# Kernel tuning notes

Hardware: AMD Instinct MI355X
Metric: run time of the kernel (lower is better)

## Reference

```python
import jax, jax.numpy as jnp
import numpy as np

EPS = 1e-5  # BatchNorm eps (eval mode, uses running stats)


def _conv1x1(x, W, b):
    # x: [B,C,H,W], W: [O,C], b: [O] -> [B,O,H,W]
    return jnp.einsum('bchw,oc->bohw', x, W) + b[None, :, None, None]


def setup_inputs() -> dict:
    key = jax.random.key(0)
    ks = jax.random.split(key, 13)
    B, C, M, N = 16, 512, 64, 64
    CR = C // 2
    s = 0.02
    return {
        'x': jax.random.normal(ks[0], (B, C, M, N), dtype=jnp.float32),
        'Wq': jax.random.normal(ks[1], (CR, C), dtype=jnp.float32) * s,
        'bq': jax.random.normal(ks[2], (CR,), dtype=jnp.float32) * s,
        'Wk': jax.random.normal(ks[3], (CR, C), dtype=jnp.float32) * s,
        'bk': jax.random.normal(ks[4], (CR,), dtype=jnp.float32) * s,
        'Wv': jax.random.normal(ks[5], (CR, C), dtype=jnp.float32) * s,
        'bv': jax.random.normal(ks[6], (CR,), dtype=jnp.float32) * s,
        'Wr': jax.random.normal(ks[7], (C, CR), dtype=jnp.float32) * s,
        'br': jax.random.normal(ks[8], (C,), dtype=jnp.float32) * s,
        'gamma': jax.random.normal(ks[9], (C,), dtype=jnp.float32) * 0.1 + 1.0,
        'beta': jax.random.normal(ks[10], (C,), dtype=jnp.float32) * 0.1,
        'running_mean': jax.random.normal(ks[11], (C,), dtype=jnp.float32) * 0.1,
        'running_var': jax.random.uniform(ks[12], (C,), dtype=jnp.float32, minval=0.5, maxval=1.5),
    }


def reference(x, Wq, bq, Wk, bk, Wv, bv, Wr, br, gamma, beta, running_mean, running_var):
    b, c, m, n = x.shape
    cr = Wq.shape[0]
    # 1x1-conv QKV projections
    Q = _conv1x1(x, Wq, bq).reshape(b * cr, m, n)
    K = _conv1x1(x, Wk, bk).reshape(b * cr, m, n)
    V = _conv1x1(x, Wv, bv).reshape(b * cr, m, n)
    # per-channel spatial attention over rows: [b*cr, m, m]
    corr = jnp.einsum('gik,gjk->gij', Q, K)
    attn = jax.nn.softmax(corr, axis=-1)
    y = jnp.einsum('gij,gjn->gin', attn, V).reshape(b, cr, m, n)
    # reconstruct: 1x1 conv + BatchNorm (eval mode) + residual
    y = _conv1x1(y, Wr, br)
    inv = gamma / jnp.sqrt(running_var + EPS)
    y = y * inv[None, :, None, None] + (beta - running_mean * inv)[None, :, None, None]
    return y + x
```

## Files before the change

### kernel.cpp

```cpp
#include <hip/hip_runtime.h>

typedef __attribute__((ext_vector_type(8))) short bf16x8;
typedef __attribute__((ext_vector_type(4))) short bf16x4;
typedef __attribute__((ext_vector_type(4))) float f32x4;

#define DEVI static __device__ __forceinline__

DEVI unsigned short f2b(float f) {
  union { float f; unsigned u; } v; v.f = f;
  unsigned r = v.u + 0x7fffu + ((v.u >> 16) & 1u);
  return (unsigned short)(r >> 16);
}

typedef const __attribute__((address_space(1))) void* gas1_t;
typedef __attribute__((address_space(3))) void* las3_t;
#define GL16(g, l) __builtin_amdgcn_global_load_lds((gas1_t)(g), (las3_t)(l), 16, 0, 0)
#define LDSOFF(p) ((unsigned)(size_t)(__attribute__((address_space(3))) void*)(p))

#define WAITVM(N) asm volatile("s_waitcnt vmcnt(" #N ")" ::: "memory")
#define WAITLGKM  asm volatile("s_waitcnt lgkmcnt(0)" ::: "memory")
#define SCHEDBAR  __builtin_amdgcn_sched_barrier(0)

#define OFF_WQKV  0ull
#define OFF_WR    786432ull
#define OFF_BQKV  1048576ull
#define OFF_SCALE 1051648ull
#define OFF_OFF2  1053696ull
#define OFF_XT    2097152ull
#define OFF_Y     35651584ull
#define OFF_Q     69206016ull

__global__ __launch_bounds__(256) void k_xt(
    const float* __restrict__ x, unsigned short* __restrict__ xt,
    const float* __restrict__ Wq, const float* __restrict__ bq,
    const float* __restrict__ Wk, const float* __restrict__ bk,
    const float* __restrict__ Wv, const float* __restrict__ bv,
    const float* __restrict__ Wr, const float* __restrict__ br,
    const float* __restrict__ gamma, const float* __restrict__ beta,
    const float* __restrict__ rm, const float* __restrict__ rv,
    unsigned short* __restrict__ wqkv, unsigned short* __restrict__ wrb,
    float* __restrict__ bqkv, float* __restrict__ scale, float* __restrict__ off2)
{
  __shared__ unsigned short tile[64][72];
  const int t = threadIdx.x;
  const int bid = blockIdx.x + blockIdx.y * 64 + blockIdx.z * 512;

  if (bid < 1536) {
    int i = bid * 256 + t;
    if (i < 768 * 512) {
      int o = i >> 9, c = i & 511;
      float v = (o < 256) ? Wq[o * 512 + c] : (o < 512 ? Wk[(o - 256) * 512 + c] : Wv[(o - 512) * 512 + c]);
      wqkv[i] = f2b(v);
    }
    if (i < 512 * 256) wrb[i] = f2b(Wr[i]);
    if (i < 768) bqkv[i] = (i < 256) ? bq[i] : (i < 512 ? bk[i - 256] : bv[i - 512]);
    if (i < 512) {
      float inv = gamma[i] * rsqrtf(rv[i] + 1e-5f);
      scale[i] = inv;
      off2[i] = (br[i] - rm[i]) * inv + beta[i];
    }
  }

  const int b = blockIdx.z, c0 = blockIdx.y * 64, s0 = blockIdx.x * 64;
  const int r = t >> 2, cc = (t & 3) * 16;
  const float* src = x + ((size_t)b * 512 + c0 + r) * 4096 + s0 + cc;
  #pragma unroll
  for (int j = 0; j < 16; j += 4) {
    float4 v = *(const float4*)(src + j);
    tile[r][cc + j + 0] = f2b(v.x);
    tile[r][cc + j + 1] = f2b(v.y);
    tile[r][cc + j + 2] = f2b(v.z);
    tile[r][cc + j + 3] = f2b(v.w);
  }
  __syncthreads();
  unsigned short* dst = xt + ((size_t)b * 4096 + s0 + r) * 512 + c0 + cc;
  bf16x8 o0, o1;
  #pragma unroll
  for (int j = 0; j < 8; ++j) { o0[j] = tile[cc + j][r]; o1[j] = tile[cc + 8 + j][r]; }
  *(bf16x8*)(dst) = o0;
  *(bf16x8*)(dst + 8) = o1;
}

__global__ __launch_bounds__(256) void k_qkv(
    const unsigned short* __restrict__ xt, const unsigned short* __restrict__ wqkv,
    const float* __restrict__ bqkv, unsigned short* __restrict__ qkv)
{
  __shared__ unsigned short lds[2][2][8192];
  const int b = blockIdx.z, o0 = blockIdx.y * 128, s0 = blockIdx.x * 128;
  const int t = threadIdx.x, w = t >> 6, l = t & 63;
  const int wm = w >> 1, wn = w & 1, lr = l & 15;
  const int lkE = (l >> 4) * 8;
  const int swE = (lr & 7) * 8;
  const int cp = (t & 7) ^ ((t >> 3) & 7);

  const unsigned short* Ag = wqkv + (size_t)(o0 + (t >> 3)) * 512 + cp * 8;
  const unsigned short* Bg = xt + ((size_t)b * 4096 + s0 + (t >> 3)) * 512 + cp * 8;

  const f32x4 z = {0.f, 0.f, 0.f, 0.f};
  f32x4 acc[4][4];
  #pragma unroll
  for (int i = 0; i < 4; ++i)
    #pragma unroll
    for (int j = 0; j < 4; ++j) acc[i][j] = z;

#define STG_Q(st, kt) do { \
    _Pragma("unroll") \
    for (int j = 0; j < 4; ++j) { \
      GL16(Ag + (kt) * 64 + j * 32 * 512, (char*)&lds[st][0][0] + j * 4096 + t * 16); \
      GL16(Bg + (kt) * 64 + j * 32 * 512, (char*)&lds[st][1][0] + j * 4096 + t * 16); \
    } \
  } while (0)

#define CMP_Q(st) do { \
    const unsigned short* A  = &lds[st][0][0]; \
    const unsigned short* Bl = &lds[st][1][0]; \
    bf16x8 af[2][4], bfr[2][4]; \
    _Pragma("unroll") \
    for (int kc = 0; kc < 2; ++kc) { \
      const int kidx = (kc * 32 + lkE) ^ swE; \
      _Pragma("unroll") \
      for (int mi = 0; mi < 4; ++mi) af[kc][mi] = *(const bf16x8*)(A + (wm * 64 + mi * 16 + lr) * 64 + kidx); \
      _Pragma("unroll") \
      for (int ni = 0; ni < 4; ++ni) bfr[kc][ni] = *(const bf16x8*)(Bl + (wn * 64 + ni * 16 + lr) * 64 + kidx); \
    } \
    _Pragma("unroll") \
    for (int kc = 0; kc < 2; ++kc) \
      _Pragma("unroll") \
      for (int mi = 0; mi < 4; ++mi) \
        _Pragma("unroll") \
        for (int ni = 0; ni < 4; ++ni) \
          acc[mi][ni] = __builtin_amdgcn_mfma_f32_16x16x32_bf16(af[kc][mi], bfr[kc][ni], acc[mi][ni], 0, 0, 0); \
  } while (0)

  STG_Q(0, 0); STG_Q(1, 1);
  #pragma unroll
  for (int kt = 0; kt < 7; ++kt) {
    WAITVM(8);
    __builtin_amdgcn_s_barrier(); SCHEDBAR;
    CMP_Q(kt & 1);
    __builtin_amdgcn_s_barrier(); SCHEDBAR;
    if (kt + 2 < 8) STG_Q(kt & 1, kt + 2);
  }
  WAITVM(0);
  __builtin_amdgcn_s_barrier(); SCHEDBAR;
  CMP_Q(1);

  #pragma unroll
  for (int mi = 0; mi < 4; ++mi) {
    #pragma unroll
    for (int reg = 0; reg < 4; ++reg) {
      const int o = o0 + wm * 64 + mi * 16 + (l >> 4) * 4 + reg;
      const float bias = bqkv[o];
      const size_t base = (size_t)(o >> 8) * 16777216ull + ((size_t)b * 256 + (o & 255)) * 4096;
      #pragma unroll
      for (int ni = 0; ni < 4; ++ni) {
        const int s = s0 + wn * 64 + ni * 16 + lr;
        qkv[base + s] = f2b(acc[mi][ni][reg] + bias);
      }
    }
  }
#undef STG_Q
#undef CMP_Q
}

__global__ __launch_bounds__(256) void k_attn(const unsigned short* __restrict__ qkv,
                                              unsigned short* __restrict__ yout)
{
  __shared__ unsigned short Vt[64][80];
  __shared__ unsigned short P[4][16][80];
  const int g = blockIdx.x;
  const unsigned short* qg = qkv + (size_t)g * 4096;
  const unsigned short* kg = qkv + 16777216ull + (size_t)g * 4096;
  const unsigned short* vg = qkv + 33554432ull + (size_t)g * 4096;
  const int t = threadIdx.x, w = t >> 6, l = t & 63;
  const int lr = l & 15, lk = (l >> 4) * 8;

  {
    const int j = t >> 2, c0 = (t & 3) * 16;
    bf16x8 a = *(const bf16x8*)(vg + j * 64 + c0);
    bf16x8 bb = *(const bf16x8*)(vg + j * 64 + c0 + 8);
    #pragma unroll
    for (int jj = 0; jj < 8; ++jj) { Vt[c0 + jj][j] = a[jj]; Vt[c0 + 8 + jj][j] = bb[jj]; }
  }

  const f32x4 z = {0.f, 0.f, 0.f, 0.f};
  bf16x8 qf[2];
  #pragma unroll
  for (int kc = 0; kc < 2; ++kc) qf[kc] = *(const bf16x8*)(qg + (w * 16 + lr) * 64 + kc * 32 + lk);
  f32x4 accS[4] = {z, z, z, z};
  __builtin_amdgcn_s_setprio(1);
  #pragma unroll
  for (int jt = 0; jt < 4; ++jt)
    #pragma unroll
    for (int kc = 0; kc < 2; ++kc) {
      bf16x8 kf = *(const bf16x8*)(kg + (jt * 16 + lr) * 64 + kc * 32 + lk);
      accS[jt] = __builtin_amdgcn_mfma_f32_16x16x32_bf16(qf[kc], kf, accS[jt], 0, 0, 0);
    }
  __builtin_amdgcn_s_setprio(0);

  #pragma unroll
  for (int reg = 0; reg < 4; ++reg) {
    float mx = fmaxf(fmaxf(accS[0][reg], accS[1][reg]), fmaxf(accS[2][reg], accS[3][reg]));
    #pragma unroll
    for (int m = 1; m < 16; m <<= 1) mx = fmaxf(mx, __shfl_xor(mx, m, 64));
    float e0 = __expf(accS[0][reg] - mx), e1 = __expf(accS[1][reg] - mx);
    float e2 = __expf(accS[2][reg] - mx), e3 = __expf(accS[3][reg] - mx);
    float sm = e0 + e1 + e2 + e3;
    #pragma unroll
    for (int m = 1; m < 16; m <<= 1) sm += __shfl_xor(sm, m, 64);
    const float rs = 1.f / sm;
    const int row = (l >> 4) * 4 + reg;
    P[w][row][0 * 16 + lr] = f2b(e0 * rs);
    P[w][row][1 * 16 + lr] = f2b(e1 * rs);
    P[w][row][2 * 16 + lr] = f2b(e2 * rs);
    P[w][row][3 * 16 + lr] = f2b(e3 * rs);
  }
  __syncthreads();

  bf16x8 pf[2];
  #pragma unroll
  for (int kc = 0; kc < 2; ++kc) pf[kc] = *(const bf16x8*)(&P[w][lr][kc * 32 + lk]);
  f32x4 accY[4] = {z, z, z, z};
  __builtin_amdgcn_s_setprio(1);
  #pragma unroll
  for (int nt = 0; nt < 4; ++nt)
    #pragma unroll
    for (int kc = 0; kc < 2; ++kc) {
      bf16x8 vf = *(const bf16x8*)(&Vt[nt * 16 + lr][kc * 32 + lk]);
      accY[nt] = __builtin_amdgcn_mfma_f32_16x16x32_bf16(pf[kc], vf, accY[nt], 0, 0, 0);
    }
  __builtin_amdgcn_s_setprio(0);

  unsigned short* yg = yout + (size_t)g * 4096;
  #pragma unroll
  for (int nt = 0; nt < 4; ++nt)
    #pragma unroll
    for (int reg = 0; reg < 4; ++reg) {
      const int i = w * 16 + (l >> 4) * 4 + reg;
      yg[i * 64 + nt * 16 + lr] = f2b(accY[nt][reg]);
    }
}

__global__ __launch_bounds__(256) void k_recon(
    const unsigned short* __restrict__ y, const unsigned short* __restrict__ wrb,
    const float* __restrict__ scale, const float* __restrict__ off2,
    const float* __restrict__ x, float* __restrict__ out)
{
  __shared__ unsigned short Albuf[2][8192];
  __shared__ unsigned short Blbuf[2][8192];
  const int b = blockIdx.z, o0 = blockIdx.y * 128, s0 = blockIdx.x * 128;
  const int t = threadIdx.x, w = t >> 6, l = t & 63;
  const int wm = w >> 1, wn = w & 1, lr = l & 15, g = l >> 4;
  const int lkE = g * 8;
  const int swE = (lr & 7) * 8;
  const int cp = (t & 7) ^ ((t >> 3) & 7);

  const unsigned short* Ag = wrb + (size_t)(o0 + (t >> 3)) * 256 + cp * 8;
  const unsigned short* Bg = y + ((size_t)b * 256 + (t >> 2)) * 4096 + s0 + (t & 3) * 32;
  const int bwbase = (t >> 4) * 1024 + (t & 3) * 256 + ((t >> 2) & 3) * 32;
  const int trbase = g * 2048 + wn * 512 + lr * 8;

  const f32x4 z = {0.f, 0.f, 0.f, 0.f};
  f32x4 acc[4][4];
  #pragma unroll
  for (int i = 0; i < 4; ++i)
    #pragma unroll
    for (int j = 0; j < 4; ++j) acc[i][j] = z;

  uint4 br0, br1, br2, br3;

#define ASTG(st, kt) do { \
    _Pragma("unroll") \
    for (int j = 0; j < 4; ++j) \
      GL16(Ag + (kt) * 64 + j * 32 * 256, (char*)&Albuf[st][0] + j * 4096 + t * 16); \
  } while (0)

#define BLOAD(kt) do { \
    br0 = *(const uint4*)(Bg + (size_t)(kt) * 64 * 4096 + 0); \
    br1 = *(const uint4*)(Bg + (size_t)(kt) * 64 * 4096 + 8); \
    br2 = *(const uint4*)(Bg + (size_t)(kt) * 64 * 4096 + 16); \
    br3 = *(const uint4*)(Bg + (size_t)(kt) * 64 * 4096 + 24); \
  } while (0)

#define BWRITE(st) do { \
    char* bp_ = (char*)&Blbuf[st][0] + bwbase; \
    *(uint4*)(bp_ + 0)   = br0; \
    *(uint4*)(bp_ + 16)  = br1; \
    *(uint4*)(bp_ + 128) = br2; \
    *(uint4*)(bp_ + 144) = br3; \
  } while (0)

#define TR2(dst, k0, k1) do { \
    bf16x4 t0_, t1_; \
    asm volatile("ds_read_b64_tr_b16 %0, %1 offset:" #k0 : "=v"(t0_) : "v"(ta)); \
    asm volatile("ds_read_b64_tr_b16 %0, %1 offset:" #k1 : "=v"(t1_) : "v"(ta)); \
    (dst) = __builtin_shufflevector(t0_, t1_, 0, 1, 2, 3, 4, 5, 6, 7); \
  } while (0)

#define CMP_R(st) do { \
    const unsigned short* A = &Albuf[st][0]; \
    unsigned ta = LDSOFF(&Blbuf[st][0]) + (unsigned)trbase; \
    bf16x8 af[2][4], bfr[2][4]; \
    _Pragma("unroll") \
    for (int kc = 0; kc < 2; ++kc) { \
      const int kidx = (kc * 32 + lkE) ^ swE; \
      _Pragma("unroll") \
      for (int mi = 0; mi < 4; ++mi) af[kc][mi] = *(const bf16x8*)(A + (wm * 64 + mi * 16 + lr) * 64 + kidx); \
    } \
    TR2(bfr[0][0], 0, 1024);    TR2(bfr[0][1], 128, 1152); \
    TR2(bfr[0][2], 256, 1280);  TR2(bfr[0][3], 384, 1408); \
    TR2(bfr[1][0], 8192, 9216); TR2(bfr[1][1], 8320, 9344); \
    TR2(bfr[1][2], 8448, 9472); TR2(bfr[1][3], 8576, 9600); \
    WAITLGKM; SCHEDBAR; \
    _Pragma("unroll") \
    for (int kc = 0; kc < 2; ++kc) \
      _Pragma("unroll") \
      for (int mi = 0; mi < 4; ++mi) \
        _Pragma("unroll") \
        for (int ni = 0; ni < 4; ++ni) \
          acc[mi][ni] = __builtin_amdgcn_mfma_f32_16x16x32_bf16(af[kc][mi], bfr[kc][ni], acc[mi][ni], 0, 0, 0); \
  } while (0)

  ASTG(0, 0); BLOAD(0); ASTG(1, 1);
  WAITVM(4);
  BWRITE(0); BLOAD(1);
  WAITLGKM;
  __builtin_amdgcn_s_barrier(); SCHEDBAR;
  CMP_R(0);
  __builtin_amdgcn_s_barrier(); SCHEDBAR;
  ASTG(0, 2);
  WAITVM(4);
  BWRITE(1); BLOAD(2);
  WAITLGKM;
  __builtin_amdgcn_s_barrier(); SCHEDBAR;
  CMP_R(1);
  __builtin_amdgcn_s_barrier(); SCHEDBAR;
  ASTG(1, 3);
  WAITVM(4);
  BWRITE(0); BLOAD(3);
  WAITLGKM;
  __builtin_amdgcn_s_barrier(); SCHEDBAR;
  CMP_R(0);
  __builtin_amdgcn_s_barrier(); SCHEDBAR;
  WAITVM(0);
  BWRITE(1);
  WAITLGKM;
  __builtin_amdgcn_s_barrier(); SCHEDBAR;
  CMP_R(1);

  const int lrow = (l >> 4) * 4;
  float xr0[16], xr1[16];

#define XLOAD(dstarr, mi) do { \
    _Pragma("unroll") \
    for (int reg = 0; reg < 4; ++reg) { \
      const int o_ = o0 + wm * 64 + (mi) * 16 + lrow + reg; \
      const size_t base_ = ((size_t)b * 512 + o_) * 4096; \
      _Pragma("unroll") \
      for (int ni = 0; ni < 4; ++ni) \
        dstarr[reg * 4 + ni] = x[base_ + s0 + wn * 64 + ni * 16 + lr]; \
    } \
  } while (0)

#define XSTORE(srcarr, mi) do { \
    _Pragma("unroll") \
    for (int reg = 0; reg < 4; ++reg) { \
      const int o_ = o0 + wm * 64 + (mi) * 16 + lrow + reg; \
      const float sc_ = scale[o_], of_ = off2[o_]; \
      const size_t base_ = ((size_t)b * 512 + o_) * 4096; \
      _Pragma("unroll") \
      for (int ni = 0; ni < 4; ++ni) { \
        const size_t idx_ = base_ + s0 + wn * 64 + ni * 16 + lr; \
        out[idx_] = acc[mi][ni][reg] * sc_ + of_ + srcarr[reg * 4 + ni]; \
      } \
    } \
  } while (0)

  XLOAD(xr0, 0);
  XLOAD(xr1, 1); SCHEDBAR;
  XSTORE(xr0, 0);
  XLOAD(xr0, 2); SCHEDBAR;
  XSTORE(xr1, 1);
  XLOAD(xr1, 3); SCHEDBAR;
  XSTORE(xr0, 2);
  XSTORE(xr1, 3);
#undef XLOAD
#undef XSTORE
#undef ASTG
#undef BLOAD
#undef BWRITE
#undef TR2
#undef CMP_R
}

extern "C" void kernel_launch(void* const* d_in, const int* in_sizes, int n_in,
                              void* d_out, int out_size, void* d_ws, size_t ws_size,
                              hipStream_t stream)
{
  const float* x     = (const float*)d_in[0];
  const float* Wq    = (const float*)d_in[1];
  const float* bq    = (const float*)d_in[2];
  const float* Wk    = (const float*)d_in[3];
  const float* bk    = (const float*)d_in[4];
  const float* Wv    = (const float*)d_in[5];
  const float* bv    = (const float*)d_in[6];
  const float* Wr    = (const float*)d_in[7];
  const float* br    = (const float*)d_in[8];
  const float* gamma = (const float*)d_in[9];
  const float* beta  = (const float*)d_in[10];
  const float* rm    = (const float*)d_in[11];
  const float* rv    = (const float*)d_in[12];

  char* ws = (char*)d_ws;
  unsigned short* wqkv  = (unsigned short*)(ws + OFF_WQKV);
  unsigned short* wrb   = (unsigned short*)(ws + OFF_WR);
  float* bqkv  = (float*)(ws + OFF_BQKV);
  float* scale = (float*)(ws + OFF_SCALE);
  float* off2  = (float*)(ws + OFF_OFF2);
  unsigned short* xt  = (unsigned short*)(ws + OFF_XT);
  unsigned short* yb  = (unsigned short*)(ws + OFF_Y);
  unsigned short* qkv = (unsigned short*)(ws + OFF_Q);
  float* out = (float*)d_out;

  hipLaunchKernelGGL(k_xt, dim3(64, 8, 16), dim3(256), 0, stream,
                     x, xt, Wq, bq, Wk, bk, Wv, bv, Wr, br, gamma, beta, rm, rv,
                     wqkv, wrb, bqkv, scale, off2);
  hipLaunchKernelGGL(k_qkv, dim3(32, 6, 16), dim3(256), 0, stream, xt, wqkv, bqkv, qkv);
  hipLaunchKernelGGL(k_attn, dim3(4096), dim3(256), 0, stream, qkv, yb);
  hipLaunchKernelGGL(k_recon, dim3(32, 4, 16), dim3(256), 0, stream, yb, wrb, scale, off2, x, out);
}
```

Measured before the change: 196.0 us.

## Fuse x transpose and bf16 conversion into QKV GEMM via LDS transpose reads

```diff
diff --git a/kernel.cpp b/kernel.cpp
--- a/kernel.cpp
+++ b/kernel.cpp
@@ -10,6 +10,9 @@
   union { float f; unsigned u; } v; v.f = f;
   unsigned r = v.u + 0x7fffu + ((v.u >> 16) & 1u);
   return (unsigned short)(r >> 16);
+}
+DEVI unsigned pk2(float lo, float hi) {
+  return (unsigned)f2b(lo) | ((unsigned)f2b(hi) << 16);
 }
 
 typedef const __attribute__((address_space(1))) void* gas1_t;
@@ -26,12 +29,10 @@
 #define OFF_BQKV  1048576ull
 #define OFF_SCALE 1051648ull
 #define OFF_OFF2  1053696ull
-#define OFF_XT    2097152ull
 #define OFF_Y     35651584ull
 #define OFF_Q     69206016ull
 
-__global__ __launch_bounds__(256) void k_xt(
-    const float* __restrict__ x, unsigned short* __restrict__ xt,
+__global__ __launch_bounds__(256) void k_prep(
     const float* __restrict__ Wq, const float* __restrict__ bq,
     const float* __restrict__ Wk, const float* __restrict__ bk,
     const float* __restrict__ Wv, const float* __restrict__ bv,
@@ -41,60 +42,38 @@
     unsigned short* __restrict__ wqkv, unsigned short* __restrict__ wrb,
     float* __restrict__ bqkv, float* __restrict__ scale, float* __restrict__ off2)
 {
-  __shared__ unsigned short tile[64][72];
-  const int t = threadIdx.x;
-  const int bid = blockIdx.x + blockIdx.y * 64 + blockIdx.z * 512;
-
-  if (bid < 1536) {
-    int i = bid * 256 + t;
-    if (i < 768 * 512) {
-      int o = i >> 9, c = i & 511;
-      float v = (o < 256) ? Wq[o * 512 + c] : (o < 512 ? Wk[(o - 256) * 512 + c] : Wv[(o - 512) * 512 + c]);
-      wqkv[i] = f2b(v);
-    }
-    if (i < 512 * 256) wrb[i] = f2b(Wr[i]);
-    if (i < 768) bqkv[i] = (i < 256) ? bq[i] : (i < 512 ? bk[i - 256] : bv[i - 512]);
-    if (i < 512) {
-      float inv = gamma[i] * rsqrtf(rv[i] + 1e-5f);
-      scale[i] = inv;
-      off2[i] = (br[i] - rm[i]) * inv + beta[i];
-    }
-  }
-
-  const int b = blockIdx.z, c0 = blockIdx.y * 64, s0 = blockIdx.x * 64;
-  const int r = t >> 2, cc = (t & 3) * 16;
-  const float* src = x + ((size_t)b * 512 + c0 + r) * 4096 + s0 + cc;
-  #pragma unroll
-  for (int j = 0; j < 16; j += 4) {
-    float4 v = *(const float4*)(src + j);
-    tile[r][cc + j + 0] = f2b(v.x);
-    tile[r][cc + j + 1] = f2b(v.y);
-    tile[r][cc + j + 2] = f2b(v.z);
-    tile[r][cc + j + 3] = f2b(v.w);
-  }
-  __syncthreads();
-  unsigned short* dst = xt + ((size_t)b * 4096 + s0 + r) * 512 + c0 + cc;
-  bf16x8 o0, o1;
-  #pragma unroll
-  for (int j = 0; j < 8; ++j) { o0[j] = tile[cc + j][r]; o1[j] = tile[cc + 8 + j][r]; }
-  *(bf16x8*)(dst) = o0;
-  *(bf16x8*)(dst + 8) = o1;
+  int i = blockIdx.x * 256 + threadIdx.x;
+  if (i < 768 * 512) {
+    int o = i >> 9, c = i & 511;
+    float v = (o < 256) ? Wq[o * 512 + c] : (o < 512 ? Wk[(o - 256) * 512 + c] : Wv[(o - 512) * 512 + c]);
+    wqkv[i] = f2b(v);
+  }
+  if (i < 512 * 256) wrb[i] = f2b(Wr[i]);
+  if (i < 768) bqkv[i] = (i < 256) ? bq[i] : (i < 512 ? bk[i - 256] : bv[i - 512]);
+  if (i < 512) {
+    float inv = gamma[i] * rsqrtf(rv[i] + 1e-5f);
+    scale[i] = inv;
+    off2[i] = (br[i] - rm[i]) * inv + beta[i];
+  }
 }
 
 __global__ __launch_bounds__(256) void k_qkv(
-    const unsigned short* __restrict__ xt, const unsigned short* __restrict__ wqkv,
+    const float* __restrict__ x, const unsigned short* __restrict__ wqkv,
     const float* __restrict__ bqkv, unsigned short* __restrict__ qkv)
 {
-  __shared__ unsigned short lds[2][2][8192];
+  __shared__ unsigned short Albuf[2][8192];
+  __shared__ unsigned short Blbuf[2][8192];
   const int b = blockIdx.z, o0 = blockIdx.y * 128, s0 = blockIdx.x * 128;
   const int t = threadIdx.x, w = t >> 6, l = t & 63;
-  const int wm = w >> 1, wn = w & 1, lr = l & 15;
-  const int lkE = (l >> 4) * 8;
+  const int wm = w >> 1, wn = w & 1, lr = l & 15, g = l >> 4;
+  const int lkE = g * 8;
   const int swE = (lr & 7) * 8;
   const int cp = (t & 7) ^ ((t >> 3) & 7);
 
   const unsigned short* Ag = wqkv + (size_t)(o0 + (t >> 3)) * 512 + cp * 8;
-  const unsigned short* Bg = xt + ((size_t)b * 4096 + s0 + (t >> 3)) * 512 + cp * 8;
+  const float* Bg = x + ((size_t)b * 512 + (t >> 2)) * 4096 + s0 + (t & 3) * 32;
+  const int bwbase = (t >> 4) * 1024 + (t & 3) * 256 + ((t >> 2) & 3) * 32;
+  const int trbase = g * 2048 + wn * 512 + lr * 8;
 
   const f32x4 z = {0.f, 0.f, 0.f, 0.f};
   f32x4 acc[4][4];
@@ -103,26 +82,56 @@
     #pragma unroll
     for (int j = 0; j < 4; ++j) acc[i][j] = z;
 
-#define STG_Q(st, kt) do { \
-    _Pragma("unroll") \
-    for (int j = 0; j < 4; ++j) { \
-      GL16(Ag + (kt) * 64 + j * 32 * 512, (char*)&lds[st][0][0] + j * 4096 + t * 16); \
-      GL16(Bg + (kt) * 64 + j * 32 * 512, (char*)&lds[st][1][0] + j * 4096 + t * 16); \
-    } \
+  float4 fr0, fr1, fr2, fr3, fr4, fr5, fr6, fr7;
+
+#define ASTG(st, kt) do { \
+    _Pragma("unroll") \
+    for (int j = 0; j < 4; ++j) \
+      GL16(Ag + (kt) * 64 + j * 32 * 512, (char*)&Albuf[st][0] + j * 4096 + t * 16); \
+  } while (0)
+
+#define BLOAD(kt) do { \
+    const float* bp_ = Bg + (size_t)(kt) * 64 * 4096; \
+    fr0 = *(const float4*)(bp_ + 0);  fr1 = *(const float4*)(bp_ + 4); \
+    fr2 = *(const float4*)(bp_ + 8);  fr3 = *(const float4*)(bp_ + 12); \
+    fr4 = *(const float4*)(bp_ + 16); fr5 = *(const float4*)(bp_ + 20); \
+    fr6 = *(const float4*)(bp_ + 24); fr7 = *(const float4*)(bp_ + 28); \
+  } while (0)
+
+#define BWRITE(st) do { \
+    char* bp_ = (char*)&Blbuf[st][0] + bwbase; \
+    uint4 c0_ = { pk2(fr0.x, fr0.y), pk2(fr0.z, fr0.w), pk2(fr1.x, fr1.y), pk2(fr1.z, fr1.w) }; \
+    uint4 c1_ = { pk2(fr2.x, fr2.y), pk2(fr2.z, fr2.w), pk2(fr3.x, fr3.y), pk2(fr3.z, fr3.w) }; \
+    uint4 c2_ = { pk2(fr4.x, fr4.y), pk2(fr4.z, fr4.w), pk2(fr5.x, fr5.y), pk2(fr5.z, fr5.w) }; \
+    uint4 c3_ = { pk2(fr6.x, fr6.y), pk2(fr6.z, fr6.w), pk2(fr7.x, fr7.y), pk2(fr7.z, fr7.w) }; \
+    *(uint4*)(bp_ + 0)   = c0_; \
+    *(uint4*)(bp_ + 16)  = c1_; \
+    *(uint4*)(bp_ + 128) = c2_; \
+    *(uint4*)(bp_ + 144) = c3_; \
+  } while (0)
+
+#define TR2(dst, k0, k1) do { \
+    bf16x4 t0_, t1_; \
+    asm volatile("ds_read_b64_tr_b16 %0, %1 offset:" #k0 : "=v"(t0_) : "v"(ta)); \
+    asm volatile("ds_read_b64_tr_b16 %0, %1 offset:" #k1 : "=v"(t1_) : "v"(ta)); \
+    (dst) = __builtin_shufflevector(t0_, t1_, 0, 1, 2, 3, 4, 5, 6, 7); \
   } while (0)
 
 #define CMP_Q(st) do { \
-    const unsigned short* A  = &lds[st][0][0]; \
-    const unsigned short* Bl = &lds[st][1][0]; \
+    const unsigned short* A = &Albuf[st][0]; \
+    unsigned ta = LDSOFF(&Blbuf[st][0]) + (unsigned)trbase; \
     bf16x8 af[2][4], bfr[2][4]; \
     _Pragma("unroll") \
     for (int kc = 0; kc < 2; ++kc) { \
       const int kidx = (kc * 32 + lkE) ^ swE; \
       _Pragma("unroll") \
       for (int mi = 0; mi < 4; ++mi) af[kc][mi] = *(const bf16x8*)(A + (wm * 64 + mi * 16 + lr) * 64 + kidx); \
-      _Pragma("unroll") \
-      for (int ni = 0; ni < 4; ++ni) bfr[kc][ni] = *(const bf16x8*)(Bl + (wn * 64 + ni * 16 + lr) * 64 + kidx); \
     } \
+    TR2(bfr[0][0], 0, 1024);    TR2(bfr[0][1], 128, 1152); \
+    TR2(bfr[0][2], 256, 1280);  TR2(bfr[0][3], 384, 1408); \
+    TR2(bfr[1][0], 8192, 9216); TR2(bfr[1][1], 8320, 9344); \
+    TR2(bfr[1][2], 8448, 9472); TR2(bfr[1][3], 8576, 9600); \
+    WAITLGKM; SCHEDBAR; \
     _Pragma("unroll") \
     for (int kc = 0; kc < 2; ++kc) \
       _Pragma("unroll") \
@@ -132,16 +141,27 @@
           acc[mi][ni] = __builtin_amdgcn_mfma_f32_16x16x32_bf16(af[kc][mi], bfr[kc][ni], acc[mi][ni], 0, 0, 0); \
   } while (0)
 
-  STG_Q(0, 0); STG_Q(1, 1);
-  #pragma unroll
-  for (int kt = 0; kt < 7; ++kt) {
-    WAITVM(8);
-    __builtin_amdgcn_s_barrier(); SCHEDBAR;
+  ASTG(0, 0); BLOAD(0); ASTG(1, 1);
+  WAITVM(4);
+  BWRITE(0); BLOAD(1);
+  WAITLGKM;
+  __builtin_amdgcn_s_barrier(); SCHEDBAR;
+  #pragma unroll
+  for (int kt = 0; kt < 6; ++kt) {
     CMP_Q(kt & 1);
     __builtin_amdgcn_s_barrier(); SCHEDBAR;
-    if (kt + 2 < 8) STG_Q(kt & 1, kt + 2);
-  }
+    ASTG(kt & 1, kt + 2);
+    WAITVM(4);
+    BWRITE((kt + 1) & 1);
+    BLOAD(kt + 2);
+    WAITLGKM;
+    __builtin_amdgcn_s_barrier(); SCHEDBAR;
+  }
+  CMP_Q(0);
+  __builtin_amdgcn_s_barrier(); SCHEDBAR;
   WAITVM(0);
+  BWRITE(1);
+  WAITLGKM;
   __builtin_amdgcn_s_barrier(); SCHEDBAR;
   CMP_Q(1);
 
@@ -159,7 +179,10 @@
       }
     }
   }
-#undef STG_Q
+#undef ASTG
+#undef BLOAD
+#undef BWRITE
+#undef TR2
 #undef CMP_Q
 }
 
@@ -417,15 +440,14 @@
   float* bqkv  = (float*)(ws + OFF_BQKV);
   float* scale = (float*)(ws + OFF_SCALE);
   float* off2  = (float*)(ws + OFF_OFF2);
-  unsigned short* xt  = (unsigned short*)(ws + OFF_XT);
   unsigned short* yb  = (unsigned short*)(ws + OFF_Y);
   unsigned short* qkv = (unsigned short*)(ws + OFF_Q);
   float* out = (float*)d_out;
 
-  hipLaunchKernelGGL(k_xt, dim3(64, 8, 16), dim3(256), 0, stream,
-                     x, xt, Wq, bq, Wk, bk, Wv, bv, Wr, br, gamma, beta, rm, rv,
+  hipLaunchKernelGGL(k_prep, dim3(1536), dim3(256), 0, stream,
+                     Wq, bq, Wk, bk, Wv, bv, Wr, br, gamma, beta, rm, rv,
                      wqkv, wrb, bqkv, scale, off2);
-  hipLaunchKernelGGL(k_qkv, dim3(32, 6, 16), dim3(256), 0, stream, xt, wqkv, bqkv, qkv);
+  hipLaunchKernelGGL(k_qkv, dim3(32, 6, 16), dim3(256), 0, stream, x, wqkv, bqkv, qkv);
   hipLaunchKernelGGL(k_attn, dim3(4096), dim3(256), 0, stream, qkv, yb);
   hipLaunchKernelGGL(k_recon, dim3(32, 4, 16), dim3(256), 0, stream, yb, wrb, scale, off2, x, out);
 }
```

After: 247.8 us. 26.4% more time.
